# Kernel tuning notes

Measured on AMD Instinct MI355X. Metric: run time of the kernel, lower is better.

## Reference

```python
import jax, jax.numpy as jnp
import numpy as np

S, N, C = 16384, 2048, 8  # n_samples, n_channels, n_components

def setup_inputs() -> dict:
    key = jax.random.key(0)
    k1, k2, k3, k4 = jax.random.split(key, 4)
    return {
        "inputs": jax.random.uniform(k1, (S, N), dtype=jnp.float32),
        "components": jax.random.uniform(k2, (C, N), dtype=jnp.float32),
        "contributions": jax.random.uniform(k3, (S, C), dtype=jnp.float32),
        "shift": jax.random.normal(k4, (S, C), dtype=jnp.float32) * 3.0,
    }

def reference(inputs, components, contributions, shift):
    # fit_shift=True branch. The original builds k_matrix[i,j] = j - i and
    # coeff[i,j] = clip(1 - |shift - (j - i)|, 0, 1), then dots with the
    # component. That is exactly linear interpolation of component at
    # position i + shift, with zero padding outside [0, N-1].
    n_samples, n_channels = inputs.shape
    n_comp = components.shape[0]
    i = jnp.arange(n_channels, dtype=shift.dtype)
    pos = i[None, None, :] + shift[:, :, None]            # [S, C, N]
    j0f = jnp.floor(pos)
    frac = pos - j0f                                      # in [0, 1)
    j0 = j0f.astype(jnp.int32)
    j1 = j0 + 1
    cidx = jnp.arange(n_comp)[None, :, None]              # broadcast over [S, C, N]
    g0 = components[cidx, jnp.clip(j0, 0, n_channels - 1)]
    g1 = components[cidx, jnp.clip(j1, 0, n_channels - 1)]
    v0 = ((j0 >= 0) & (j0 < n_channels)).astype(components.dtype)
    v1 = ((j1 >= 0) & (j1 < n_channels)).astype(components.dtype)
    shifted = g0 * (1.0 - frac) * v0 + g1 * frac * v1     # [S, C, N] shifted components
    # scale by per-sample contributions and sum over components
    return jnp.einsum('scn,sc->sn', shifted, contributions)
```

## Files before the change

kernel.cpp:

```cpp
#include <hip/hip_runtime.h>
#include <hip/hip_fp16.h>


namespace {
constexpr int kS     = 16384;
constexpr int kN     = 2048;
constexpr int kC     = 8;
constexpr int kM     = 16;
constexpr int kBlock = 256;
constexpr int kPadH  = 32;
constexpr int kUnits = 1057;
constexpr int kRowStride = 1192;

__device__ __forceinline__ int swz(int u) { return u + (u >> 3); }

__global__ __launch_bounds__(kBlock, 4)
void smf_kernel(const float* __restrict__ comps,
                const float* __restrict__ contrib,
                const float* __restrict__ shift,
                float* __restrict__ out)
{
    __shared__ uint32_t ldsU[kC * kRowStride];

    const int tid = threadIdx.x;

    for (int c = 0; c < kC; ++c) {
        const float* src = comps + c * kN;
        uint32_t* dst = ldsU + c * kRowStride;
        for (int u = tid; u < kUnits; u += kBlock) {
            const int j = 2 * u - kPadH;
            float2 v = make_float2(0.f, 0.f);
            if (j >= 0 && j < kN - 1) v = *reinterpret_cast<const float2*>(src + j);
            __half2 h2 = __floats2half2_rn(v.x, v.y);
            dst[swz(u)] = *reinterpret_cast<const uint32_t*>(&h2);
        }
    }
    __syncthreads();

    const int s0 = blockIdx.x * kM;
    const int n0 = tid * 8;

    float4 cA = *reinterpret_cast<const float4*>(contrib + (size_t)s0 * kC);
    float4 cB = *reinterpret_cast<const float4*>(contrib + (size_t)s0 * kC + 4);
    float4 sA = *reinterpret_cast<const float4*>(shift   + (size_t)s0 * kC);
    float4 sB = *reinterpret_cast<const float4*>(shift   + (size_t)s0 * kC + 4);

    #pragma unroll 1
    for (int si = 0; si < kM; ++si) {
        const int s = s0 + si;
        const float4 ccA = cA, ccB = cB, csA = sA, csB = sB;
        const int sn = (si + 1 < kM) ? (s + 1) : s;
        cA = *reinterpret_cast<const float4*>(contrib + (size_t)sn * kC);
        cB = *reinterpret_cast<const float4*>(contrib + (size_t)sn * kC + 4);
        sA = *reinterpret_cast<const float4*>(shift   + (size_t)sn * kC);
        sB = *reinterpret_cast<const float4*>(shift   + (size_t)sn * kC + 4);

        const float ct[8] = {ccA.x, ccA.y, ccA.z, ccA.w, ccB.x, ccB.y, ccB.z, ccB.w};
        const float sh[8] = {csA.x, csA.y, csA.z, csA.w, csB.x, csB.y, csB.z, csB.w};

        float acc[8];
        #pragma unroll
        for (int k = 0; k < 8; ++k) acc[k] = 0.f;

        #pragma unroll
        for (int c = 0; c < kC; ++c) {
            const float fl = floorf(sh[c]);
            const float fr = sh[c] - fl;
            int d = (int)fl;
            d = d < -31 ? -31 : (d > 31 ? 31 : d);
            const float w1 = ct[c] * fr;
            const float w0 = ct[c] - w1;

            const int a   = n0 + d + kPadH;
            const int u0  = a >> 1;
            const bool odd = (a & 1) != 0;

            const uint32_t* row = ldsU + c * kRowStride;
            const uint32_t y0 = row[swz(u0 + 0)];
            const uint32_t y1 = row[swz(u0 + 1)];
            const uint32_t y2 = row[swz(u0 + 2)];
            const uint32_t y3 = row[swz(u0 + 3)];
            const uint32_t y4 = row[swz(u0 + 4)];
            const uint32_t y5 = row[swz(u0 + 5)];

            const uint32_t z0 = odd ? __builtin_amdgcn_alignbit(y1, y0, 16) : y0;
            const uint32_t z1 = odd ? __builtin_amdgcn_alignbit(y2, y1, 16) : y1;
            const uint32_t z2 = odd ? __builtin_amdgcn_alignbit(y3, y2, 16) : y2;
            const uint32_t z3 = odd ? __builtin_amdgcn_alignbit(y4, y3, 16) : y3;
            const uint32_t z4 = odd ? __builtin_amdgcn_alignbit(y5, y4, 16) : y4;

            const float2 f0 = __half22float2(*reinterpret_cast<const __half2*>(&z0));
            const float2 f1 = __half22float2(*reinterpret_cast<const __half2*>(&z1));
            const float2 f2 = __half22float2(*reinterpret_cast<const __half2*>(&z2));
            const float2 f3 = __half22float2(*reinterpret_cast<const __half2*>(&z3));
            const float2 f4 = __half22float2(*reinterpret_cast<const __half2*>(&z4));

            acc[0] += w0 * f0.x + w1 * f0.y;
            acc[1] += w0 * f0.y + w1 * f1.x;
            acc[2] += w0 * f1.x + w1 * f1.y;
            acc[3] += w0 * f1.y + w1 * f2.x;
            acc[4] += w0 * f2.x + w1 * f2.y;
            acc[5] += w0 * f2.y + w1 * f3.x;
            acc[6] += w0 * f3.x + w1 * f3.y;
            acc[7] += w0 * f3.y + w1 * f4.x;
        }

        float4* orow = reinterpret_cast<float4*>(out + (size_t)s * kN + n0);
        orow[0] = make_float4(acc[0], acc[1], acc[2], acc[3]);
        orow[1] = make_float4(acc[4], acc[5], acc[6], acc[7]);
    }
}
}

extern "C" void kernel_launch(void* const* d_in, const int* in_sizes, int n_in,
                              void* d_out, int out_size, void* d_ws, size_t ws_size,
                              hipStream_t stream) {
    const float* comps   = (const float*)d_in[1];
    const float* contrib = (const float*)d_in[2];
    const float* shiftp  = (const float*)d_in[3];
    float* out = (float*)d_out;

    dim3 grid(kS / kM);
    dim3 block(kBlock);
    smf_kernel<<<grid, block, 0, stream>>>(comps, contrib, shiftp, out);
}
```

Baseline: 297.4 us.

## Use 64-bit LDS reads, drop swizzle, and run four sample groups per block

The bank-conflict swizzle is removed and the staged half2 component rows are read with three 64-bit LDS loads instead of six 32-bit loads. A word-select plus a variable alignbit shift recovers the unaligned 16-bit window. The block grows to 1024 threads split into four groups of 256, each handling eight samples, so each LDS fill is reused by 32 samples. The next-sample prefetch of contrib/shift is dropped. Risks: unswizzled 64-bit reads may cause bank conflicts, and the aggressive launch bounds may constrain registers, while fewer, larger blocks leave fewer blocks per CU.

```diff
diff --git a/kernel.cpp b/kernel.cpp
--- a/kernel.cpp
+++ b/kernel.cpp
@@ -6,88 +6,81 @@
 constexpr int kS     = 16384;
 constexpr int kN     = 2048;
 constexpr int kC     = 8;
-constexpr int kM     = 16;
-constexpr int kBlock = 256;
+constexpr int kM     = 32;
+constexpr int kBlock = 1024;
 constexpr int kPadH  = 32;
-constexpr int kUnits = 1057;
-constexpr int kRowStride = 1192;
+constexpr int kRowW  = 1064;
 
-__device__ __forceinline__ int swz(int u) { return u + (u >> 3); }
-
-__global__ __launch_bounds__(kBlock, 4)
+__global__ __launch_bounds__(kBlock, 8)
 void smf_kernel(const float* __restrict__ comps,
                 const float* __restrict__ contrib,
                 const float* __restrict__ shift,
                 float* __restrict__ out)
 {
-    __shared__ uint32_t ldsU[kC * kRowStride];
+    __shared__ alignas(16) uint32_t ldsU[kC * kRowW];
 
     const int tid = threadIdx.x;
 
     for (int c = 0; c < kC; ++c) {
         const float* src = comps + c * kN;
-        uint32_t* dst = ldsU + c * kRowStride;
-        for (int u = tid; u < kUnits; u += kBlock) {
+        uint32_t* dst = ldsU + c * kRowW;
+        for (int u = tid; u < kRowW; u += kBlock) {
             const int j = 2 * u - kPadH;
             float2 v = make_float2(0.f, 0.f);
-            if (j >= 0 && j < kN - 1) v = *reinterpret_cast<const float2*>(src + j);
-            __half2 h2 = __floats2half2_rn(v.x, v.y);
-            dst[swz(u)] = *reinterpret_cast<const uint32_t*>(&h2);
+            if (j >= 0 && j < kN) v = *reinterpret_cast<const float2*>(src + j);
+            const __half2 h2 = __floats2half2_rn(v.x, v.y);
+            dst[u] = *reinterpret_cast<const uint32_t*>(&h2);
         }
     }
     __syncthreads();
 
-    const int s0 = blockIdx.x * kM;
-    const int n0 = tid * 8;
-
-    float4 cA = *reinterpret_cast<const float4*>(contrib + (size_t)s0 * kC);
-    float4 cB = *reinterpret_cast<const float4*>(contrib + (size_t)s0 * kC + 4);
-    float4 sA = *reinterpret_cast<const float4*>(shift   + (size_t)s0 * kC);
-    float4 sB = *reinterpret_cast<const float4*>(shift   + (size_t)s0 * kC + 4);
+    const int grp   = tid >> 8;
+    const int n0    = (tid & 255) * 8;
+    const int sBase = blockIdx.x * kM + grp * (kM / 4);
 
     #pragma unroll 1
-    for (int si = 0; si < kM; ++si) {
-        const int s = s0 + si;
-        const float4 ccA = cA, ccB = cB, csA = sA, csB = sB;
-        const int sn = (si + 1 < kM) ? (s + 1) : s;
-        cA = *reinterpret_cast<const float4*>(contrib + (size_t)sn * kC);
-        cB = *reinterpret_cast<const float4*>(contrib + (size_t)sn * kC + 4);
-        sA = *reinterpret_cast<const float4*>(shift   + (size_t)sn * kC);
-        sB = *reinterpret_cast<const float4*>(shift   + (size_t)sn * kC + 4);
+    for (int si = 0; si < kM / 4; ++si) {
+        const int s = sBase + si;
+        const float4 cA = *reinterpret_cast<const float4*>(contrib + (size_t)s * kC);
+        const float4 cB = *reinterpret_cast<const float4*>(contrib + (size_t)s * kC + 4);
+        const float4 sA = *reinterpret_cast<const float4*>(shift   + (size_t)s * kC);
+        const float4 sB = *reinterpret_cast<const float4*>(shift   + (size_t)s * kC + 4);
+        const float ct[8] = {cA.x, cA.y, cA.z, cA.w, cB.x, cB.y, cB.z, cB.w};
+        const float sh[8] = {sA.x, sA.y, sA.z, sA.w, sB.x, sB.y, sB.z, sB.w};
 
-        const float ct[8] = {ccA.x, ccA.y, ccA.z, ccA.w, ccB.x, ccB.y, ccB.z, ccB.w};
-        const float sh[8] = {csA.x, csA.y, csA.z, csA.w, csB.x, csB.y, csB.z, csB.w};
-
-        float acc[8];
-        #pragma unroll
-        for (int k = 0; k < 8; ++k) acc[k] = 0.f;
+        float acc[8] = {0.f, 0.f, 0.f, 0.f, 0.f, 0.f, 0.f, 0.f};
 
         #pragma unroll
         for (int c = 0; c < kC; ++c) {
             const float fl = floorf(sh[c]);
             const float fr = sh[c] - fl;
             int d = (int)fl;
-            d = d < -31 ? -31 : (d > 31 ? 31 : d);
+            d = d < -kPadH ? -kPadH : (d > 39 ? 39 : d);
             const float w1 = ct[c] * fr;
             const float w0 = ct[c] - w1;
 
-            const int a   = n0 + d + kPadH;
-            const int u0  = a >> 1;
-            const bool odd = (a & 1) != 0;
+            const int a = n0 + d + kPadH;
+            const int e = (a >> 1) & ~1;
+            const uint32_t* p64 = ldsU + c * kRowW + e;
 
-            const uint32_t* row = ldsU + c * kRowStride;
-            const uint32_t y0 = row[swz(u0 + 0)];
-            const uint32_t y1 = row[swz(u0 + 1)];
-            const uint32_t y2 = row[swz(u0 + 2)];
-            const uint32_t y3 = row[swz(u0 + 3)];
-            const uint32_t y4 = row[swz(u0 + 4)];
-            const uint32_t y5 = row[swz(u0 + 5)];
+            const uint2 q0 = *reinterpret_cast<const uint2*>(p64);
+            const uint2 q1 = *reinterpret_cast<const uint2*>(p64 + 2);
+            const uint2 q2 = *reinterpret_cast<const uint2*>(p64 + 4);
 
-            const uint32_t z0 = odd ? __builtin_amdgcn_alignbit(y1, y0, 16) : y0;
-            const uint32_t z1 = odd ? __builtin_amdgcn_alignbit(y2, y1, 16) : y1;
-            const uint32_t z2 = odd ? __builtin_amdgcn_alignbit(y3, y2, 16) : y2;
-            const uint32_t z3 = odd ? __builtin_amdgcn_alignbit(y4, y3, 16) : y3;
-            const uint32_t z4 = odd ? __builtin_amdgcn_alignbit(y5, y4, 16) : y4;
+            const bool    wsel = ((a >> 1) & 1) != 0;
+            const uint32_t shp = (uint32_t)(a & 1) << 4;
+
+            const uint32_t t0 = wsel ? q0.y : q0.x;
+            const uint32_t t1 = wsel ? q1.x : q0.y;
+            const uint32_t t2 = wsel ? q1.y : q1.x;
+            const uint32_t t3 = wsel ? q2.x : q1.y;
+            const uint32_t t4 = wsel ? q2.y : q2.x;
+
+            const uint32_t z0 = __builtin_amdgcn_alignbit(t1, t0, shp);
+            const uint32_t z1 = __builtin_amdgcn_alignbit(t2, t1, shp);
+            const uint32_t z2 = __builtin_amdgcn_alignbit(t3, t2, shp);
+            const uint32_t z3 = __builtin_amdgcn_alignbit(t4, t3, shp);
+            const uint32_t z4 = __builtin_amdgcn_alignbit(t4, t4, shp);
 
             const float2 f0 = __half22float2(*reinterpret_cast<const __half2*>(&z0));
             const float2 f1 = __half22float2(*reinterpret_cast<const __half2*>(&z1));
```

Result: slower. 325.6 us (+9.5%).
